# Performance work log

Measured on AMD Instinct MI355X. Metric: run time of the kernel, lower is better.

## Reference

```python
import jax, jax.numpy as jnp
import numpy as np

B, C_IN, C_OUT, N = 4096, 256, 256, 25


def setup_inputs() -> dict:
    key = jax.random.key(0)
    k_x, k_adj, k_w, k_b = jax.random.split(key, 4)
    x = jax.random.normal(k_x, (B, C_IN, N), dtype=jnp.float32)
    adj = jax.random.uniform(k_adj, (N, N), dtype=jnp.float32)
    # Conv1d(C_in, C_out, 1) weight is [C_out, C_in, 1]; drop trailing 1.
    W = jax.random.normal(k_w, (C_OUT, C_IN), dtype=jnp.float32) * (1.0 / np.sqrt(C_IN))
    b = jax.random.normal(k_b, (C_OUT,), dtype=jnp.float32) * 0.01
    return {"x": x, "adj": adj, "W": W, "b": b}


def reference(x, adj, W, b):
    # 1x1 Conv1d == per-node linear transform: [B, C_out, N]
    support = jnp.einsum('oc,bcn->bon', W, x) + b[None, :, None]
    # Dense adjacency aggregation: support @ adj.T -> [B, C_out, N]
    output = jnp.einsum('bon,mn->bom', support, adj)
    # dropout=0 (disabled); in_features == out_features -> identity residual
    return jax.nn.relu(output + x)
```

## Files before the change

### kernel.cpp

```cpp
#include <hip/hip_runtime.h>
#include <hip/hip_bf16.h>


#define BATCH 4096
#define C 256
#define N 25
#define NB 8
#define XSTR 28
#define YSTR 264

typedef __bf16 bf16x8 __attribute__((ext_vector_type(8)));
typedef float f32x4 __attribute__((ext_vector_type(4)));

__global__ void prep_kernel(const float* __restrict__ W, const float* __restrict__ adj,
                            bf16x8* __restrict__ Wshuf, float* __restrict__ adjS) {
    int i = blockIdx.x * 256 + threadIdx.x;
    int f = i >> 6, l = i & 63;
    int wv = f >> 5, kk = (f >> 2) & 7, ot = f & 3;
    int quad = l >> 4, l15 = l & 15;
    int o = wv * 64 + ot * 16 + l15;
    int cb = kk * 32 + quad * 8;
    bf16x8 v;
    #pragma unroll
    for (int j = 0; j < 8; ++j) v[j] = (__bf16)W[o * C + cb + j];
    Wshuf[i] = v;
    if (blockIdx.x == 0 && threadIdx.x < 32) {
        float s = 0.f;
        if (threadIdx.x < N)
            for (int n = 0; n < N; ++n) s += adj[threadIdx.x * N + n];
        adjS[threadIdx.x] = s;
    }
}

__global__ __launch_bounds__(256, 2) void gcn_kernel(
    const float* __restrict__ x, const float* __restrict__ adj,
    const float* __restrict__ bias, const float* __restrict__ adjSg,
    const bf16x8* __restrict__ Wshuf, float* __restrict__ out)
{
    __shared__ __align__(16) float  xs[C * XSTR];
    __shared__ __align__(16) __bf16 ys[32 * YSTR];
    __shared__ __align__(16) __bf16 adjbf[32 * 40];
    __shared__ __align__(16) float  outS[C * N];
    __shared__ float biasS[C];

    const int tid = threadIdx.x;
    const int wv = tid >> 6, lane = tid & 63;
    const int quad = lane >> 4, l15 = lane & 15;
    const int o0 = wv * 64;
    const int b0 = blockIdx.x * NB;

    for (int e = tid; e < N * N; e += 256) {
        int m = e / N, n = e - m * N;
        adjbf[m * 40 + n] = (__bf16)adj[e];
    }
    if (tid < N) {
        #pragma unroll
        for (int n = N; n < 32; ++n) adjbf[tid * 40 + n] = (__bf16)0.f;
    } else if (tid < 32) {
        #pragma unroll
        for (int n = 0; n < 32; ++n) adjbf[tid * 40 + n] = (__bf16)0.f;
    }
    biasS[tid] = bias[tid];

    bf16x8 af[8][4];
    #pragma unroll
    for (int kk = 0; kk < 8; ++kk)
        #pragma unroll
        for (int ot = 0; ot < 4; ++ot)
            af[kk][ot] = Wshuf[((wv * 8 + kk) * 4 + ot) * 64 + lane];

    const float aS0 = adjSg[l15];
    const float aS1 = adjSg[16 + l15];

    __syncthreads();

    const bf16x8 a0 = *(const bf16x8*)&adjbf[l15 * 40 + quad * 8];
    const bf16x8 a1 = *(const bf16x8*)&adjbf[(16 + l15) * 40 + quad * 8];

    #pragma unroll 1
    for (int bi = 0; bi < NB; ++bi) {
        const float* xb = x + (size_t)(b0 + bi) * (C * N);
        float* outb = out + (size_t)(b0 + bi) * (C * N);

        #pragma unroll
        for (int q = 0; q < 7; ++q) {
            int i4 = q * 256 + tid;
            if (i4 < (C * N) / 4) {
                float4 v = ((const float4*)xb)[i4];
                int e = i4 * 4;
                int c = e / N, n = e - c * N;
                float fv[4] = {v.x, v.y, v.z, v.w};
                #pragma unroll
                for (int j = 0; j < 4; ++j) {
                    xs[c * XSTR + n] = fv[j];
                    ++n; if (n == N) { n = 0; ++c; }
                }
            }
        }
        __syncthreads();

        f32x4 yacc[4][2];
        #pragma unroll
        for (int ctl = 0; ctl < 4; ++ctl) {
            const int c = o0 + ctl * 16 + l15;
            bf16x8 xf;
            if (quad < 3) {
                f32x4 u = *(const f32x4*)&xs[c * XSTR + quad * 8];
                f32x4 w = *(const f32x4*)&xs[c * XSTR + quad * 8 + 4];
                xf[0] = (__bf16)u[0]; xf[1] = (__bf16)u[1]; xf[2] = (__bf16)u[2]; xf[3] = (__bf16)u[3];
                xf[4] = (__bf16)w[0]; xf[5] = (__bf16)w[1]; xf[6] = (__bf16)w[2]; xf[7] = (__bf16)w[3];
            } else {
                float u = xs[c * XSTR + 24];
                xf[0] = (__bf16)u;
                #pragma unroll
                for (int j = 1; j < 8; ++j) xf[j] = (__bf16)0.f;
            }
            yacc[ctl][0] = __builtin_amdgcn_mfma_f32_16x16x32_bf16(a0, xf, (f32x4)0.f, 0, 0, 0);
            yacc[ctl][1] = __builtin_amdgcn_mfma_f32_16x16x32_bf16(a1, xf, (f32x4)0.f, 0, 0, 0);
        }
        #pragma unroll
        for (int ctl = 0; ctl < 4; ++ctl) {
            const int c = o0 + ctl * 16 + l15;
            #pragma unroll
            for (int mt = 0; mt < 2; ++mt)
                #pragma unroll
                for (int r = 0; r < 4; ++r)
                    ys[(mt * 16 + quad * 4 + r) * YSTR + c] = (__bf16)yacc[ctl][mt][r];
        }
        __syncthreads();

        f32x4 acc[4][2];
        #pragma unroll
        for (int ot = 0; ot < 4; ++ot) { acc[ot][0] = (f32x4)0.f; acc[ot][1] = (f32x4)0.f; }
        #pragma unroll
        for (int kk = 0; kk < 8; ++kk) {
            bf16x8 bfr0 = *(const bf16x8*)&ys[l15 * YSTR + kk * 32 + quad * 8];
            bf16x8 bfr1 = *(const bf16x8*)&ys[(16 + l15) * YSTR + kk * 32 + quad * 8];
            #pragma unroll
            for (int ot = 0; ot < 4; ++ot) {
                acc[ot][0] = __builtin_amdgcn_mfma_f32_16x16x32_bf16(af[kk][ot], bfr0, acc[ot][0], 0, 0, 0);
                acc[ot][1] = __builtin_amdgcn_mfma_f32_16x16x32_bf16(af[kk][ot], bfr1, acc[ot][1], 0, 0, 0);
            }
        }

        #pragma unroll
        for (int ot = 0; ot < 4; ++ot)
            #pragma unroll
            for (int r = 0; r < 4; ++r) {
                const int o = o0 + ot * 16 + quad * 4 + r;
                const float bia = biasS[o];
                {
                    const int m = l15;
                    float v = acc[ot][0][r] + bia * aS0 + xs[o * XSTR + m];
                    outS[o * N + m] = v > 0.f ? v : 0.f;
                }
                if (l15 < N - 16) {
                    const int m = 16 + l15;
                    float v = acc[ot][1][r] + bia * aS1 + xs[o * XSTR + m];
                    outS[o * N + m] = v > 0.f ? v : 0.f;
                }
            }
        __syncthreads();

        #pragma unroll
        for (int q = 0; q < 7; ++q) {
            int i4 = q * 256 + tid;
            if (i4 < (C * N) / 4)
                ((float4*)outb)[i4] = ((const float4*)outS)[i4];
        }
    }
}

extern "C" void kernel_launch(void* const* d_in, const int* in_sizes, int n_in,
                              void* d_out, int out_size, void* d_ws, size_t ws_size,
                              hipStream_t stream) {
    (void)in_sizes; (void)n_in; (void)out_size; (void)ws_size;
    const float* x    = (const float*)d_in[0];
    const float* adj  = (const float*)d_in[1];
    const float* W    = (const float*)d_in[2];
    const float* bias = (const float*)d_in[3];
    float* out = (float*)d_out;

    unsigned char* ws = (unsigned char*)d_ws;
    bf16x8* Wshuf = (bf16x8*)ws;
    float*  adjS  = (float*)(ws + 131072);

    prep_kernel<<<32, 256, 0, stream>>>(W, adj, Wshuf, adjS);
    gcn_kernel<<<BATCH / NB, 256, 0, stream>>>(x, adj, bias, adjS, Wshuf, out);
}
```

Measured before the change: 231.8 us.

## Prefetch next batch into registers, reuse xs as output buffer, stream W from L2

```diff
diff --git a/kernel.cpp b/kernel.cpp
--- a/kernel.cpp
+++ b/kernel.cpp
@@ -5,9 +5,10 @@
 #define BATCH 4096
 #define C 256
 #define N 25
-#define NB 8
+#define NB 4
 #define XSTR 28
 #define YSTR 264
+#define NCH 7
 
 typedef __bf16 bf16x8 __attribute__((ext_vector_type(8)));
 typedef float f32x4 __attribute__((ext_vector_type(4)));
@@ -32,7 +33,7 @@
     }
 }
 
-__global__ __launch_bounds__(256, 2) void gcn_kernel(
+__global__ __launch_bounds__(256, 3) void gcn_kernel(
     const float* __restrict__ x, const float* __restrict__ adj,
     const float* __restrict__ bias, const float* __restrict__ adjSg,
     const bf16x8* __restrict__ Wshuf, float* __restrict__ out)
@@ -40,7 +41,6 @@
     __shared__ __align__(16) float  xs[C * XSTR];
     __shared__ __align__(16) __bf16 ys[32 * YSTR];
     __shared__ __align__(16) __bf16 adjbf[32 * 40];
-    __shared__ __align__(16) float  outS[C * N];
     __shared__ float biasS[C];
 
     const int tid = threadIdx.x;
@@ -49,6 +49,16 @@
     const int o0 = wv * 64;
     const int b0 = blockIdx.x * NB;
 
+    float4 pf[NCH];
+    {
+        const float4* xb4 = (const float4*)(x + (size_t)b0 * (C * N));
+        #pragma unroll
+        for (int q = 0; q < NCH; ++q) {
+            int i4 = q * 256 + tid;
+            if (i4 < (C * N) / 4) pf[q] = xb4[i4];
+        }
+    }
+
     for (int e = tid; e < N * N; e += 256) {
         int m = e / N, n = e - m * N;
         adjbf[m * 40 + n] = (__bf16)adj[e];
@@ -61,17 +71,8 @@
         for (int n = 0; n < 32; ++n) adjbf[tid * 40 + n] = (__bf16)0.f;
     }
     biasS[tid] = bias[tid];
-
-    bf16x8 af[8][4];
-    #pragma unroll
-    for (int kk = 0; kk < 8; ++kk)
-        #pragma unroll
-        for (int ot = 0; ot < 4; ++ot)
-            af[kk][ot] = Wshuf[((wv * 8 + kk) * 4 + ot) * 64 + lane];
-
     const float aS0 = adjSg[l15];
     const float aS1 = adjSg[16 + l15];
-
     __syncthreads();
 
     const bf16x8 a0 = *(const bf16x8*)&adjbf[l15 * 40 + quad * 8];
@@ -79,94 +80,124 @@
 
     #pragma unroll 1
     for (int bi = 0; bi < NB; ++bi) {
-        const float* xb = x + (size_t)(b0 + bi) * (C * N);
-        float* outb = out + (size_t)(b0 + bi) * (C * N);
-
-        #pragma unroll
-        for (int q = 0; q < 7; ++q) {
+        {
+            float4* outp = (float4*)(out + (size_t)(b0 + bi - 1) * (C * N));
+            #pragma unroll
+            for (int q = 0; q < NCH; ++q) {
+                int i4 = q * 256 + tid;
+                if (i4 < (C * N) / 4) {
+                    int e = i4 * 4;
+                    int cc = e / N, nn = e - cc * N;
+                    int addr = cc * XSTR + nn;
+                    float fv[4] = {pf[q].x, pf[q].y, pf[q].z, pf[q].w};
+                    float rv[4];
+                    #pragma unroll
+                    for (int j = 0; j < 4; ++j) {
+                        rv[j] = xs[addr];
+                        xs[addr] = fv[j];
+                        ++nn; ++addr;
+                        if (nn == N) { nn = 0; addr += XSTR - N; }
+                    }
+                    if (bi > 0) outp[i4] = make_float4(rv[0], rv[1], rv[2], rv[3]);
+                }
+            }
+        }
+        if (bi + 1 < NB) {
+            const float4* xn4 = (const float4*)(x + (size_t)(b0 + bi + 1) * (C * N));
+            #pragma unroll
+            for (int q = 0; q < NCH; ++q) {
+                int i4 = q * 256 + tid;
+                if (i4 < (C * N) / 4) pf[q] = xn4[i4];
+            }
+        }
+        __syncthreads();
+
+        {
+            f32x4 yacc[4][2];
+            #pragma unroll
+            for (int ctl = 0; ctl < 4; ++ctl) {
+                const int c = o0 + ctl * 16 + l15;
+                bf16x8 xf;
+                if (quad < 3) {
+                    f32x4 u = *(const f32x4*)&xs[c * XSTR + quad * 8];
+                    f32x4 w = *(const f32x4*)&xs[c * XSTR + quad * 8 + 4];
+                    xf[0] = (__bf16)u[0]; xf[1] = (__bf16)u[1]; xf[2] = (__bf16)u[2]; xf[3] = (__bf16)u[3];
+                    xf[4] = (__bf16)w[0]; xf[5] = (__bf16)w[1]; xf[6] = (__bf16)w[2]; xf[7] = (__bf16)w[3];
+                } else {
+                    float u = xs[c * XSTR + 24];
+                    xf[0] = (__bf16)u;
+                    #pragma unroll
+                    for (int j = 1; j < 8; ++j) xf[j] = (__bf16)0.f;
+                }
+                yacc[ctl][0] = __builtin_amdgcn_mfma_f32_16x16x32_bf16(a0, xf, (f32x4)0.f, 0, 0, 0);
+                yacc[ctl][1] = __builtin_amdgcn_mfma_f32_16x16x32_bf16(a1, xf, (f32x4)0.f, 0, 0, 0);
+            }
+            #pragma unroll
+            for (int ctl = 0; ctl < 4; ++ctl) {
+                const int c = o0 + ctl * 16 + l15;
+                #pragma unroll
+                for (int mt = 0; mt < 2; ++mt)
+                    #pragma unroll
+                    for (int r = 0; r < 4; ++r)
+                        ys[(mt * 16 + quad * 4 + r) * YSTR + c] = (__bf16)yacc[ctl][mt][r];
+            }
+        }
+        __syncthreads();
+
+        {
+            f32x4 acc[4][2];
+            #pragma unroll
+            for (int ot = 0; ot < 4; ++ot) { acc[ot][0] = (f32x4)0.f; acc[ot][1] = (f32x4)0.f; }
+            #pragma unroll
+            for (int kk = 0; kk < 8; ++kk) {
+                bf16x8 bfr0 = *(const bf16x8*)&ys[l15 * YSTR + kk * 32 + quad * 8];
+                bf16x8 bfr1 = *(const bf16x8*)&ys[(16 + l15) * YSTR + kk * 32 + quad * 8];
+                #pragma unroll
+                for (int ot = 0; ot < 4; ++ot) {
+                    bf16x8 af = Wshuf[((wv * 8 + kk) * 4 + ot) * 64 + lane];
+                    acc[ot][0] = __builtin_amdgcn_mfma_f32_16x16x32_bf16(af, bfr0, acc[ot][0], 0, 0, 0);
+                    acc[ot][1] = __builtin_amdgcn_mfma_f32_16x16x32_bf16(af, bfr1, acc[ot][1], 0, 0, 0);
+                }
+            }
+            #pragma unroll
+            for (int ot = 0; ot < 4; ++ot)
+                #pragma unroll
+                for (int r = 0; r < 4; ++r) {
+                    const int o = o0 + ot * 16 + quad * 4 + r;
+                    const float bia = biasS[o];
+                    {
+                        const int m = l15;
+                        float v = acc[ot][0][r] + bia * aS0 + xs[o * XSTR + m];
+                        xs[o * XSTR + m] = v > 0.f ? v : 0.f;
+                    }
+                    if (l15 < N - 16) {
+                        const int m = 16 + l15;
+                        float v = acc[ot][1][r] + bia * aS1 + xs[o * XSTR + m];
+                        xs[o * XSTR + m] = v > 0.f ? v : 0.f;
+                    }
+                }
+        }
+        __syncthreads();
+    }
+
+    {
+        float4* outp = (float4*)(out + (size_t)(b0 + NB - 1) * (C * N));
+        #pragma unroll
+        for (int q = 0; q < NCH; ++q) {
             int i4 = q * 256 + tid;
             if (i4 < (C * N) / 4) {
-                float4 v = ((const float4*)xb)[i4];
                 int e = i4 * 4;
-                int c = e / N, n = e - c * N;
-                float fv[4] = {v.x, v.y, v.z, v.w};
+                int cc = e / N, nn = e - cc * N;
+                int addr = cc * XSTR + nn;
+                float rv[4];
                 #pragma unroll
                 for (int j = 0; j < 4; ++j) {
-                    xs[c * XSTR + n] = fv[j];
-                    ++n; if (n == N) { n = 0; ++c; }
-                }
-            }
-        }
-        __syncthreads();
-
-        f32x4 yacc[4][2];
-        #pragma unroll
-        for (int ctl = 0; ctl < 4; ++ctl) {
-            const int c = o0 + ctl * 16 + l15;
-            bf16x8 xf;
-            if (quad < 3) {
-                f32x4 u = *(const f32x4*)&xs[c * XSTR + quad * 8];
-                f32x4 w = *(const f32x4*)&xs[c * XSTR + quad * 8 + 4];
-                xf[0] = (__bf16)u[0]; xf[1] = (__bf16)u[1]; xf[2] = (__bf16)u[2]; xf[3] = (__bf16)u[3];
-                xf[4] = (__bf16)w[0]; xf[5] = (__bf16)w[1]; xf[6] = (__bf16)w[2]; xf[7] = (__bf16)w[3];
-            } else {
-                float u = xs[c * XSTR + 24];
-                xf[0] = (__bf16)u;
-                #pragma unroll
-                for (int j = 1; j < 8; ++j) xf[j] = (__bf16)0.f;
-            }
-            yacc[ctl][0] = __builtin_amdgcn_mfma_f32_16x16x32_bf16(a0, xf, (f32x4)0.f, 0, 0, 0);
-            yacc[ctl][1] = __builtin_amdgcn_mfma_f32_16x16x32_bf16(a1, xf, (f32x4)0.f, 0, 0, 0);
-        }
-        #pragma unroll
-        for (int ctl = 0; ctl < 4; ++ctl) {
-            const int c = o0 + ctl * 16 + l15;
-            #pragma unroll
-            for (int mt = 0; mt < 2; ++mt)
-                #pragma unroll
-                for (int r = 0; r < 4; ++r)
-                    ys[(mt * 16 + quad * 4 + r) * YSTR + c] = (__bf16)yacc[ctl][mt][r];
-        }
-        __syncthreads();
-
-        f32x4 acc[4][2];
-        #pragma unroll
-        for (int ot = 0; ot < 4; ++ot) { acc[ot][0] = (f32x4)0.f; acc[ot][1] = (f32x4)0.f; }
-        #pragma unroll
-        for (int kk = 0; kk < 8; ++kk) {
-            bf16x8 bfr0 = *(const bf16x8*)&ys[l15 * YSTR + kk * 32 + quad * 8];
-            bf16x8 bfr1 = *(const bf16x8*)&ys[(16 + l15) * YSTR + kk * 32 + quad * 8];
-            #pragma unroll
-            for (int ot = 0; ot < 4; ++ot) {
-                acc[ot][0] = __builtin_amdgcn_mfma_f32_16x16x32_bf16(af[kk][ot], bfr0, acc[ot][0], 0, 0, 0);
-                acc[ot][1] = __builtin_amdgcn_mfma_f32_16x16x32_bf16(af[kk][ot], bfr1, acc[ot][1], 0, 0, 0);
-            }
-        }
-
-        #pragma unroll
-        for (int ot = 0; ot < 4; ++ot)
-            #pragma unroll
-            for (int r = 0; r < 4; ++r) {
-                const int o = o0 + ot * 16 + quad * 4 + r;
-                const float bia = biasS[o];
-                {
-                    const int m = l15;
-                    float v = acc[ot][0][r] + bia * aS0 + xs[o * XSTR + m];
-                    outS[o * N + m] = v > 0.f ? v : 0.f;
-                }
-                if (l15 < N - 16) {
-                    const int m = 16 + l15;
-                    float v = acc[ot][1][r] + bia * aS1 + xs[o * XSTR + m];
-                    outS[o * N + m] = v > 0.f ? v : 0.f;
-                }
-            }
-        __syncthreads();
-
-        #pragma unroll
-        for (int q = 0; q < 7; ++q) {
-            int i4 = q * 256 + tid;
-            if (i4 < (C * N) / 4)
-                ((float4*)outb)[i4] = ((const float4*)outS)[i4];
+                    rv[j] = xs[addr];
+                    ++nn; ++addr;
+                    if (nn == N) { nn = 0; addr += XSTR - N; }
+                }
+                outp[i4] = make_float4(rv[0], rv[1], rv[2], rv[3]);
+            }
         }
     }
 }
```

Measured after the change: 319.3 us. +37.7%, slower.
